# Performance work log

Hardware: AMD Instinct MI355X
Metric: run time of the kernel (lower is better)

Reference implementation:

```python
import jax, jax.numpy as jnp
import numpy as np

D_MODEL = 1024
N_HEADS = 16
D_K = D_MODEL // N_HEADS
NEG_INF = -1.0e9


def setup_inputs() -> dict:
    key = jax.random.key(0)
    ks = jax.random.split(key, 12)
    B, S = 2, 2048
    inp = {
        "q": jax.random.normal(ks[0], (B, S, D_MODEL), dtype=jnp.float32),
        "k": jax.random.normal(ks[1], (B, S, D_MODEL), dtype=jnp.float32),
        "v": jax.random.normal(ks[2], (B, S, D_MODEL), dtype=jnp.float32),
        "mask": jax.random.randint(ks[3], (B, 1, S, S), 0, 2, dtype=jnp.int32),
        "Wq": jax.random.normal(ks[4], (D_MODEL, D_MODEL), dtype=jnp.float32) / np.sqrt(D_MODEL),
        "bq": jnp.zeros((D_MODEL,), dtype=jnp.float32),
        "Wk": jax.random.normal(ks[5], (D_MODEL, D_MODEL), dtype=jnp.float32) / np.sqrt(D_MODEL),
        "bk": jnp.zeros((D_MODEL,), dtype=jnp.float32),
        "Wv": jax.random.normal(ks[6], (D_MODEL, D_MODEL), dtype=jnp.float32) / np.sqrt(D_MODEL),
        "bv": jnp.zeros((D_MODEL,), dtype=jnp.float32),
        "Wo": jax.random.normal(ks[7], (D_MODEL, D_MODEL), dtype=jnp.float32) / np.sqrt(D_MODEL),
        "bo": jnp.zeros((D_MODEL,), dtype=jnp.float32),
    }
    return inp


def _split_heads(x):
    B, S, _ = x.shape
    return x.reshape(B, S, N_HEADS, D_K).transpose(0, 2, 1, 3)  # [B,H,S,Dk]


def reference(q, k, v, mask, Wq, bq, Wk, bk, Wv, bv, Wo, bo):
    # QKV projections (nn.Linear: x @ W.T + b; here W stored as [in,out]-agnostic square)
    query = _split_heads(q @ Wq + bq)
    key_ = _split_heads(k @ Wk + bk)
    value = _split_heads(v @ Wv + bv)

    scale = 1.0 / np.sqrt(D_K).astype(np.float32)
    scores = jnp.einsum("bhqd,bhkd->bhqk", query, key_) * scale  # [B,H,S,S]
    scores = jnp.where(mask == 0, NEG_INF, scores)
    attn = jax.nn.softmax(scores, axis=-1)  # dropout is identity in eval (p=0.0)
    ctx = jnp.einsum("bhqk,bhkd->bhqd", attn, value)  # [B,H,S,Dk]

    B, H, S, Dk = ctx.shape
    ctx = ctx.transpose(0, 2, 1, 3).reshape(B, S, H * Dk)
    return ctx @ Wo + bo
```

## Files before the change

### kernel.cpp

```cpp
#include <hip/hip_runtime.h>
#include <hip/hip_bf16.h>

typedef __bf16 bf16_t;
typedef __bf16 bf16x2 __attribute__((ext_vector_type(2)));
typedef __bf16 bf16x8 __attribute__((ext_vector_type(8)));
typedef float f32x4 __attribute__((ext_vector_type(4)));
typedef float f32x16 __attribute__((ext_vector_type(16)));
typedef int intx4 __attribute__((ext_vector_type(4)));
typedef unsigned int u32;
typedef unsigned long long u64;

#define S_LEN 2048
#define DM 1024
#define NH 16
#define DK 64
#define M_ROWS 4096
#define SCALE_LOG2E 0.1803368801111204f

__device__ __forceinline__ int sw_off(int row, int col) {
  return row * 64 + ((((col >> 3) ^ row) & 7) << 3) + (col & 7);
}

__device__ __forceinline__ bf16x8 cvt8(const float4& a, const float4& b) {
  bf16x8 v;
  v[0] = (__bf16)a.x; v[1] = (__bf16)a.y; v[2] = (__bf16)a.z; v[3] = (__bf16)a.w;
  v[4] = (__bf16)b.x; v[5] = (__bf16)b.y; v[6] = (__bf16)b.z; v[7] = (__bf16)b.w;
  return v;
}

__device__ __forceinline__ void glds16(const bf16_t* g, bf16_t* l) {
  __builtin_amdgcn_global_load_lds(
      (const __attribute__((address_space(1))) void*)g,
      (__attribute__((address_space(3))) void*)l, 16, 0, 0);
}

__device__ __forceinline__ int pk2(float lo, float hi) {
  bf16x2 t;
  t[0] = (__bf16)lo;
  t[1] = (__bf16)hi;
  return __builtin_bit_cast(int, t);
}

__global__ __launch_bounds__(256) void prep(
    const float* __restrict__ q, const float* __restrict__ k,
    const float* __restrict__ v, bf16_t* __restrict__ Xb,
    const float* __restrict__ Wq, const float* __restrict__ Wk,
    const float* __restrict__ Wv, const float* __restrict__ Wo,
    bf16_t* __restrict__ Wt,
    const int* __restrict__ mask, u64* __restrict__ mb)
{
  __shared__ float tile[64][65];
  const int blk = blockIdx.x;
  if (blk < 6144) {
    const int z = blk >> 11;
    const int bx = blk & 2047;
    const float* __restrict__ src = (z == 0) ? q : ((z == 1) ? k : v);
    const size_t idx = ((size_t)bx * 256 + threadIdx.x) * 8;
    const float4 a = *(const float4*)&src[idx];
    const float4 b = *(const float4*)&src[idx + 4];
    *(bf16x8*)&Xb[(size_t)z * M_ROWS * DM + idx] = cvt8(a, b);
  } else if (blk < 7168) {
    const int idx = blk - 6144;
    const int z = idx >> 8, by = (idx >> 4) & 15, bx = idx & 15;
    const float* __restrict__ W = (z == 0) ? Wq : ((z == 1) ? Wk : ((z == 2) ? Wv : Wo));
    bf16_t* __restrict__ out = Wt + (size_t)z * DM * DM;
    const int tx = threadIdx.x & 31, ty = threadIdx.x >> 5;
    const int k0 = bx * 64, n0 = by * 64;
    #pragma unroll
    for (int j = 0; j < 8; ++j) {
      const float2 vv = *(const float2*)&W[(size_t)(k0 + ty + 8 * j) * DM + n0 + tx * 2];
      tile[ty + 8 * j][tx * 2] = vv.x;
      tile[ty + 8 * j][tx * 2 + 1] = vv.y;
    }
    __syncthreads();
    #pragma unroll
    for (int j = 0; j < 8; ++j) {
      const int a = ty + 8 * j;
      bf16x2 p;
      p[0] = (__bf16)tile[tx * 2][a];
      p[1] = (__bf16)tile[tx * 2 + 1][a];
      *(bf16x2*)&out[(size_t)(n0 + a) * DM + k0 + tx * 2] = p;
    }
  } else {
    const int wgl = (blk - 7168) * 4 + (threadIdx.x >> 6);
    const int lane = threadIdx.x & 63;
    const int qq = wgl & 2047;
    const int kw = (wgl >> 11) & 31;
    const int b = wgl >> 16;
    const int val = mask[((size_t)(b * S_LEN + qq)) * S_LEN + kw * 64 + lane];
    const u64 bits = __ballot(val != 0);
    if (lane == 0) mb[wgl] = bits;
  }
}

__device__ __forceinline__ void gemm128_body(
    const bf16_t* __restrict__ A, const bf16_t* __restrict__ Bt,
    const float* __restrict__ bias, const float scale,
    bf16_t* __restrict__ outb, float* __restrict__ outf)
{
  __shared__ __align__(16) bf16_t As[128 * 64];
  __shared__ __align__(16) bf16_t Bs[128 * 64];
  const int t = threadIdx.x, w = t >> 6, L = t & 63, quad = L >> 4, l16 = L & 15;
  const int m0 = blockIdx.x * 128, n0 = blockIdx.y * 128;
  const int mb = 64 * (w & 1), nb = 64 * (w >> 1);
  const int rowS = t >> 3;
  const int ck = (((t & 7) ^ (rowS & 7)) << 3);

  f32x4 acc[4][4] = {};
  for (int k0 = 0; k0 < DM; k0 += 64) {
    __syncthreads();
    #pragma unroll
    for (int j = 0; j < 4; ++j) {
      glds16(&A[(size_t)(m0 + 32 * j + rowS) * DM + k0 + ck],  &As[j * 2048 + t * 8]);
      glds16(&Bt[(size_t)(n0 + 32 * j + rowS) * DM + k0 + ck], &Bs[j * 2048 + t * 8]);
    }
    __syncthreads();
    #pragma unroll
    for (int kk = 0; kk < 2; ++kk) {
      bf16x8 af[4], bfr[4];
      #pragma unroll
      for (int mt = 0; mt < 4; ++mt)
        af[mt] = *(const bf16x8*)&As[sw_off(mb + 16 * mt + l16, kk * 32 + quad * 8)];
      #pragma unroll
      for (int ct = 0; ct < 4; ++ct)
        bfr[ct] = *(const bf16x8*)&Bs[sw_off(nb + 16 * ct + l16, kk * 32 + quad * 8)];
      #pragma unroll
      for (int mt = 0; mt < 4; ++mt)
        #pragma unroll
        for (int ct = 0; ct < 4; ++ct)
          acc[mt][ct] = __builtin_amdgcn_mfma_f32_16x16x32_bf16(af[mt], bfr[ct], acc[mt][ct], 0, 0, 0);
    }
  }
  #pragma unroll
  for (int mt = 0; mt < 4; ++mt)
    #pragma unroll
    for (int ct = 0; ct < 4; ++ct)
      #pragma unroll
      for (int r = 0; r < 4; ++r) {
        const int row = m0 + mb + 16 * mt + quad * 4 + r;
        const int n = n0 + nb + 16 * ct + l16;
        const float val = (acc[mt][ct][r] + bias[n]) * scale;
        if (outb) outb[(size_t)row * DM + n] = (__bf16)val;
        else      outf[(size_t)row * DM + n] = val;
      }
}

__global__ __launch_bounds__(256) void gemm_qkv(
    const bf16_t* __restrict__ Xb, const bf16_t* __restrict__ Wt,
    const float* __restrict__ bq, const float* __restrict__ bk,
    const float* __restrict__ bv, bf16_t* __restrict__ QKVb)
{
  const int z = blockIdx.z;
  gemm128_body(Xb + (size_t)z * M_ROWS * DM, Wt + (size_t)z * DM * DM,
               (z == 0) ? bq : ((z == 1) ? bk : bv),
               (z == 0) ? SCALE_LOG2E : 1.0f,
               QKVb + (size_t)z * M_ROWS * DM, nullptr);
}

__global__ __launch_bounds__(256) void gemm_out(
    const bf16_t* __restrict__ ctx, const bf16_t* __restrict__ Wto,
    const float* __restrict__ bo, float* __restrict__ out)
{
  gemm128_body(ctx, Wto, bo, 1.0f, nullptr, out);
}

__global__ __launch_bounds__(256) void transpV(
    const bf16_t* __restrict__ Vb, bf16_t* __restrict__ Vtw)
{
  __shared__ bf16_t Tr[64 * 72];
  const int t = threadIdx.x;
  const int key0 = blockIdx.x * 64;
  const int bh = blockIdx.y, b = bh >> 4, h = bh & 15;
  const int r = t >> 2, c = (t & 3) * 16;
  const bf16_t* src = &Vb[(size_t)(b * S_LEN + key0 + r) * DM + h * DK + c];
  const bf16x8 v0 = *(const bf16x8*)src;
  const bf16x8 v1 = *(const bf16x8*)(src + 8);
  #pragma unroll
  for (int j = 0; j < 8; ++j) {
    Tr[r * 72 + c + j] = v0[j];
    Tr[r * 72 + c + 8 + j] = v1[j];
  }
  __syncthreads();
  const int dv = t >> 2, kc = (t & 3) * 16;
  bf16_t ov[16];
  #pragma unroll
  for (int j = 0; j < 16; ++j) ov[j] = Tr[(kc + j) * 72 + dv];
  bf16_t* dst = &Vtw[((size_t)bh * DK + dv) * S_LEN + key0 + kc];
  *(bf16x8*)dst = *(bf16x8*)&ov[0];
  *(bf16x8*)(dst + 8) = *(bf16x8*)&ov[8];
}

__global__ __launch_bounds__(512, 2) void attn_kernel(
    const bf16_t* __restrict__ Qb, const bf16_t* __restrict__ Kb,
    const bf16_t* __restrict__ Vtw, const u64* __restrict__ mb,
    bf16_t* __restrict__ ctx)
{
  __shared__ __align__(16) bf16_t KVs[2][4][64 * 64];

  const int t = threadIdx.x, w = t >> 6, L = t & 63;
  const int l31 = L & 31, h5 = L >> 5;
  const int g = blockIdx.x;
  const int xcd = g & 7, slot = g >> 3;
  const int bh = xcd * 4 + (slot >> 3), qt = slot & 7;
  const int q0 = qt * 256;
  const int b = bh >> 4, h = bh & 15;

  const int qr = q0 + 32 * w + l31;
  bf16x8 qf[4];
  {
    const bf16_t* qsrc = &Qb[(size_t)(b * S_LEN + qr) * DM + h * DK + 8 * h5];
    #pragma unroll
    for (int ks = 0; ks < 4; ++ks) qf[ks] = *(const bf16x8*)(qsrc + 16 * ks);
  }

  const int rk = t >> 3;
  const int ck = (t & 7) ^ (rk & 7);
  const bf16_t* pK = &Kb[(size_t)(b * S_LEN + rk) * DM + h * DK + ck * 8];
  const bf16_t* pV = &Vtw[((size_t)bh * DK + rk) * S_LEN + ck * 8];
  const u64* pm = &mb[(size_t)b * 32 * S_LEN + qr];

  f32x16 O[2] = {};
  float l_lane = 0.f;

  auto compute = [&](const bf16_t* __restrict__ Kc, const bf16_t* __restrict__ Vc,
                     u64 mcur) {
    f32x16 s0 = {}, s1 = {};
    #pragma unroll
    for (int ks = 0; ks < 4; ++ks) {
      const bf16x8 kf0 = *(const bf16x8*)&Kc[sw_off(l31, ks * 16 + 8 * h5)];
      const bf16x8 kf1 = *(const bf16x8*)&Kc[sw_off(32 + l31, ks * 16 + 8 * h5)];
      s0 = __builtin_amdgcn_mfma_f32_32x32x16_bf16(kf0, qf[ks], s0, 0, 0, 0);
      s1 = __builtin_amdgcn_mfma_f32_32x32x16_bf16(kf1, qf[ks], s1, 0, 0, 0);
    }
    #pragma unroll
    for (int nt = 0; nt < 2; ++nt) {
      const u32 mm = ((u32)(mcur >> (nt ? 32 : 0))) >> (4 * h5);
      const f32x16 sacc = nt ? s1 : s0;
      float p[16];
      #pragma unroll
      for (int r = 0; r < 16; ++r) {
        const int cb = (r & 3) + 8 * (r >> 2);
        const u32 mr = (u32)(((int)(mm << (31 - cb))) >> 31);
        const float e = __builtin_exp2f(sacc[r]);
        const float pv = __builtin_bit_cast(float, __builtin_bit_cast(u32, e) & mr);
        l_lane += pv;
        p[r] = pv;
      }
      #pragma unroll
      for (int ss = 0; ss < 2; ++ss) {
        const int x0 = pk2(p[8 * ss + 0], p[8 * ss + 1]);
        const int x1 = pk2(p[8 * ss + 2], p[8 * ss + 3]);
        const int y0 = pk2(p[8 * ss + 4], p[8 * ss + 5]);
        const int y1 = pk2(p[8 * ss + 6], p[8 * ss + 7]);
        const auto r0 = __builtin_amdgcn_permlane32_swap(x0, y0, false, false);
        const auto r1 = __builtin_amdgcn_permlane32_swap(x1, y1, false, false);
        intx4 wv;
        wv[0] = r0[0]; wv[1] = r1[0]; wv[2] = r0[1]; wv[3] = r1[1];
        const bf16x8 pf = __builtin_bit_cast(bf16x8, wv);
        const int s4 = 2 * nt + ss;
        const bf16x8 vf0 = *(const bf16x8*)&Vc[sw_off(l31, s4 * 16 + 8 * h5)];
        const bf16x8 vf1 = *(const bf16x8*)&Vc[sw_off(32 + l31, s4 * 16 + 8 * h5)];
        O[0] = __builtin_amdgcn_mfma_f32_32x32x16_bf16(vf0, pf, O[0], 0, 0, 0);
        O[1] = __builtin_amdgcn_mfma_f32_32x32x16_bf16(vf1, pf, O[1], 0, 0, 0);
      }
    }
  };

  bf16x8 k0r = *(const bf16x8*)pK;
  bf16x8 k1r = *(const bf16x8*)(pK + (size_t)64 * DM);
  bf16x8 v0r = *(const bf16x8*)pV;
  bf16x8 v1r = *(const bf16x8*)(pV + 64);
  u64 m0 = pm[0], m1 = pm[S_LEN];
  pK += (size_t)128 * DM; pV += 128; pm += 2 * S_LEN;
  *(bf16x8*)&KVs[0][0][t * 8] = k0r;
  *(bf16x8*)&KVs[0][1][t * 8] = k1r;
  *(bf16x8*)&KVs[0][2][t * 8] = v0r;
  *(bf16x8*)&KVs[0][3][t * 8] = v1r;
  __syncthreads();

  for (int kt = 0; kt < S_LEN / 128; ++kt) {
    const int cur = kt & 1;
    u64 n0 = 0, n1 = 0;
    if (kt + 1 < S_LEN / 128) {
      k0r = *(const bf16x8*)pK;
      k1r = *(const bf16x8*)(pK + (size_t)64 * DM);
      v0r = *(const bf16x8*)pV;
      v1r = *(const bf16x8*)(pV + 64);
      n0 = pm[0]; n1 = pm[S_LEN];
      pK += (size_t)128 * DM; pV += 128; pm += 2 * S_LEN;
    }
    compute(&KVs[cur][0][0], &KVs[cur][2][0], m0);
    compute(&KVs[cur][1][0], &KVs[cur][3][0], m1);
    if (kt + 1 < S_LEN / 128) {
      *(bf16x8*)&KVs[cur ^ 1][0][t * 8] = k0r;
      *(bf16x8*)&KVs[cur ^ 1][1][t * 8] = k1r;
      *(bf16x8*)&KVs[cur ^ 1][2][t * 8] = v0r;
      *(bf16x8*)&KVs[cur ^ 1][3][t * 8] = v1r;
      m0 = n0; m1 = n1;
    }
    __syncthreads();
  }

  const float lsum = l_lane + __shfl_xor(l_lane, 32);
  const float inv = 1.f / lsum;
  bf16_t* sc = &KVs[0][0][0] + (size_t)w * 2048;
  #pragma unroll
  for (int ot = 0; ot < 2; ++ot)
    #pragma unroll
    for (int r = 0; r < 16; ++r) {
      const int dv = 32 * ot + (r & 3) + 8 * (r >> 2) + 4 * h5;
      sc[sw_off(l31, dv)] = (__bf16)(O[ot][r] * inv);
    }
  const int erow = L >> 1, ecol = (L & 1) * 32;
  bf16_t* dst = &ctx[(size_t)(b * S_LEN + q0 + 32 * w + erow) * DM + h * DK + ecol];
  #pragma unroll
  for (int c8 = 0; c8 < 4; ++c8)
    *(bf16x8*)(dst + 8 * c8) = *(const bf16x8*)&sc[sw_off(erow, ecol + 8 * c8)];
}

extern "C" void kernel_launch(void* const* d_in, const int* in_sizes, int n_in,
                              void* d_out, int out_size, void* d_ws, size_t ws_size,
                              hipStream_t stream) {
  const float* q  = (const float*)d_in[0];
  const float* k  = (const float*)d_in[1];
  const float* v  = (const float*)d_in[2];
  const int* mask = (const int*)d_in[3];
  const float* Wq = (const float*)d_in[4];
  const float* bq = (const float*)d_in[5];
  const float* Wk = (const float*)d_in[6];
  const float* bk = (const float*)d_in[7];
  const float* Wv = (const float*)d_in[8];
  const float* bv = (const float*)d_in[9];
  const float* Wo = (const float*)d_in[10];
  const float* bo = (const float*)d_in[11];
  float* out = (float*)d_out;

  const size_t SLICE = (size_t)M_ROWS * DM;
  bf16_t* Xb   = (bf16_t*)d_ws;
  bf16_t* QKVb = Xb + 3 * SLICE;
  bf16_t* Wt   = QKVb + 3 * SLICE;
  u64* mbw     = (u64*)(Wt + (size_t)4 * DM * DM);
  bf16_t* ctx  = Xb;
  bf16_t* Vtw  = Xb + SLICE;

  prep<<<dim3(39936), dim3(256), 0, stream>>>(q, k, v, Xb, Wq, Wk, Wv, Wo, Wt,
                                              mask, mbw);
  gemm_qkv<<<dim3(32, 8, 3), dim3(256), 0, stream>>>(Xb, Wt, bq, bk, bv, QKVb);
  transpV<<<dim3(32, 32), dim3(256), 0, stream>>>(QKVb + 2 * SLICE, Vtw);
  attn_kernel<<<dim3(256), dim3(512), 0, stream>>>(QKVb, QKVb + SLICE, Vtw, mbw, ctx);
  gemm_out<<<dim3(32, 8), dim3(256), 0, stream>>>(ctx, Wt + (size_t)3 * DM * DM, bo, out);
}
```

Baseline: 288.9 us.

## Fuse V transpose into QKV GEMM, vectorize mask packing, retile GEMMs

The separate V-transpose kernel is removed: the V projection now transposes its tile through shared memory and writes the head-transposed layout directly. Mask bit-packing switches from one wavefront ballot per 64 keys to one thread per 64 keys using int4 loads, which cuts the prep grid size. The QKV GEMM drops to a K-step of 32 with an unswizzled LDS layout, and the output GEMM gets a 64x128 tile to launch more blocks. The unswizzled LDS reads may cause bank conflicts, and the smaller K-step doubles the number of barriers.

```diff
diff --git a/kernel.cpp b/kernel.cpp
--- a/kernel.cpp
+++ b/kernel.cpp
@@ -3,6 +3,7 @@
 
 typedef __bf16 bf16_t;
 typedef __bf16 bf16x2 __attribute__((ext_vector_type(2)));
+typedef __bf16 bf16x4 __attribute__((ext_vector_type(4)));
 typedef __bf16 bf16x8 __attribute__((ext_vector_type(8)));
 typedef float f32x4 __attribute__((ext_vector_type(4)));
 typedef float f32x16 __attribute__((ext_vector_type(16)));
@@ -82,55 +83,85 @@
       *(bf16x2*)&out[(size_t)(n0 + a) * DM + k0 + tx * 2] = p;
     }
   } else {
-    const int wgl = (blk - 7168) * 4 + (threadIdx.x >> 6);
-    const int lane = threadIdx.x & 63;
-    const int qq = wgl & 2047;
-    const int kw = (wgl >> 11) & 31;
-    const int b = wgl >> 16;
-    const int val = mask[((size_t)(b * S_LEN + qq)) * S_LEN + kw * 64 + lane];
-    const u64 bits = __ballot(val != 0);
-    if (lane == 0) mb[wgl] = bits;
+    const int g = (blk - 7168) * 256 + threadIdx.x;
+    const int qq = g & 2047;
+    const int kw = (g >> 11) & 31;
+    const int b = g >> 16;
+    const int* src = &mask[((size_t)(b * S_LEN + qq)) * S_LEN + kw * 64];
+    u64 bits = 0;
+    #pragma unroll
+    for (int i = 0; i < 16; ++i) {
+      const int4 m4 = *(const int4*)&src[i * 4];
+      bits |= (u64)(m4.x != 0) << (4 * i);
+      bits |= (u64)(m4.y != 0) << (4 * i + 1);
+      bits |= (u64)(m4.z != 0) << (4 * i + 2);
+      bits |= (u64)(m4.w != 0) << (4 * i + 3);
+    }
+    mb[g] = bits;
   }
 }
 
 __device__ __forceinline__ void gemm128_body(
     const bf16_t* __restrict__ A, const bf16_t* __restrict__ Bt,
     const float* __restrict__ bias, const float scale,
-    bf16_t* __restrict__ outb, float* __restrict__ outf)
-{
-  __shared__ __align__(16) bf16_t As[128 * 64];
-  __shared__ __align__(16) bf16_t Bs[128 * 64];
+    bf16_t* __restrict__ outb, float* __restrict__ outf,
+    bf16_t* __restrict__ vtw)
+{
+  __shared__ __align__(16) bf16_t Smem[128 * 136];
+  bf16_t* As = Smem;
+  bf16_t* Bs = Smem + 4096;
   const int t = threadIdx.x, w = t >> 6, L = t & 63, quad = L >> 4, l16 = L & 15;
   const int m0 = blockIdx.x * 128, n0 = blockIdx.y * 128;
   const int mb = 64 * (w & 1), nb = 64 * (w >> 1);
-  const int rowS = t >> 3;
-  const int ck = (((t & 7) ^ (rowS & 7)) << 3);
+  const int rowS = t >> 2, subS = (t & 3) * 8;
 
   f32x4 acc[4][4] = {};
-  for (int k0 = 0; k0 < DM; k0 += 64) {
-    __syncthreads();
-    #pragma unroll
-    for (int j = 0; j < 4; ++j) {
-      glds16(&A[(size_t)(m0 + 32 * j + rowS) * DM + k0 + ck],  &As[j * 2048 + t * 8]);
-      glds16(&Bt[(size_t)(n0 + 32 * j + rowS) * DM + k0 + ck], &Bs[j * 2048 + t * 8]);
-    }
-    __syncthreads();
-    #pragma unroll
-    for (int kk = 0; kk < 2; ++kk) {
-      bf16x8 af[4], bfr[4];
-      #pragma unroll
-      for (int mt = 0; mt < 4; ++mt)
-        af[mt] = *(const bf16x8*)&As[sw_off(mb + 16 * mt + l16, kk * 32 + quad * 8)];
+  for (int k0 = 0; k0 < DM; k0 += 32) {
+    __syncthreads();
+    glds16(&A[(size_t)(m0 + rowS) * DM + k0 + subS],        &As[t * 8]);
+    glds16(&A[(size_t)(m0 + 64 + rowS) * DM + k0 + subS],   &As[2048 + t * 8]);
+    glds16(&Bt[(size_t)(n0 + rowS) * DM + k0 + subS],       &Bs[t * 8]);
+    glds16(&Bt[(size_t)(n0 + 64 + rowS) * DM + k0 + subS],  &Bs[2048 + t * 8]);
+    __syncthreads();
+    bf16x8 af[4], bfr[4];
+    #pragma unroll
+    for (int mt = 0; mt < 4; ++mt)
+      af[mt] = *(const bf16x8*)&As[(mb + 16 * mt + l16) * 32 + quad * 8];
+    #pragma unroll
+    for (int ct = 0; ct < 4; ++ct)
+      bfr[ct] = *(const bf16x8*)&Bs[(nb + 16 * ct + l16) * 32 + quad * 8];
+    #pragma unroll
+    for (int mt = 0; mt < 4; ++mt)
       #pragma unroll
       for (int ct = 0; ct < 4; ++ct)
-        bfr[ct] = *(const bf16x8*)&Bs[sw_off(nb + 16 * ct + l16, kk * 32 + quad * 8)];
-      #pragma unroll
-      for (int mt = 0; mt < 4; ++mt)
+        acc[mt][ct] = __builtin_amdgcn_mfma_f32_16x16x32_bf16(af[mt], bfr[ct], acc[mt][ct], 0, 0, 0);
+  }
+
+  if (vtw) {
+    __syncthreads();
+    #pragma unroll
+    for (int mt = 0; mt < 4; ++mt)
+      #pragma unroll
+      for (int ct = 0; ct < 4; ++ct) {
+        const int nloc = nb + 16 * ct + l16;
+        const int mloc0 = mb + 16 * mt + quad * 4;
+        bf16x4 pk;
         #pragma unroll
-        for (int ct = 0; ct < 4; ++ct)
-          acc[mt][ct] = __builtin_amdgcn_mfma_f32_16x16x32_bf16(af[mt], bfr[ct], acc[mt][ct], 0, 0, 0);
-    }
-  }
+        for (int r = 0; r < 4; ++r)
+          pk[r] = (__bf16)(acc[mt][ct][r] + bias[n0 + nloc]);
+        *(bf16x4*)&Smem[nloc * 136 + mloc0] = pk;
+      }
+    __syncthreads();
+    const int nloc = t >> 1, mh = (t & 1) * 64;
+    const int n = n0 + nloc, h = n >> 6, dv = n & 63;
+    const int b = m0 >> 11, key0 = (m0 & 2047) + mh;
+    bf16_t* dst = &vtw[(((size_t)(b * NH + h)) * DK + dv) * S_LEN + key0];
+    #pragma unroll
+    for (int j = 0; j < 8; ++j)
+      *(bf16x8*)(dst + 8 * j) = *(const bf16x8*)&Smem[nloc * 136 + mh + 8 * j];
+    return;
+  }
+
   #pragma unroll
   for (int mt = 0; mt < 4; ++mt)
     #pragma unroll
@@ -148,46 +179,58 @@
 __global__ __launch_bounds__(256) void gemm_qkv(
     const bf16_t* __restrict__ Xb, const bf16_t* __restrict__ Wt,
     const float* __restrict__ bq, const float* __restrict__ bk,
-    const float* __restrict__ bv, bf16_t* __restrict__ QKVb)
+    const float* __restrict__ bv, bf16_t* __restrict__ QKVb,
+    bf16_t* __restrict__ Vtw)
 {
   const int z = blockIdx.z;
   gemm128_body(Xb + (size_t)z * M_ROWS * DM, Wt + (size_t)z * DM * DM,
                (z == 0) ? bq : ((z == 1) ? bk : bv),
                (z == 0) ? SCALE_LOG2E : 1.0f,
-               QKVb + (size_t)z * M_ROWS * DM, nullptr);
+               (z == 2) ? nullptr : QKVb + (size_t)z * M_ROWS * DM, nullptr,
+               (z == 2) ? Vtw : nullptr);
 }
 
 __global__ __launch_bounds__(256) void gemm_out(
-    const bf16_t* __restrict__ ctx, const bf16_t* __restrict__ Wto,
-    const float* __restrict__ bo, float* __restrict__ out)
-{
-  gemm128_body(ctx, Wto, bo, 1.0f, nullptr, out);
-}
-
-__global__ __launch_bounds__(256) void transpV(
-    const bf16_t* __restrict__ Vb, bf16_t* __restrict__ Vtw)
-{
-  __shared__ bf16_t Tr[64 * 72];
-  const int t = threadIdx.x;
-  const int key0 = blockIdx.x * 64;
-  const int bh = blockIdx.y, b = bh >> 4, h = bh & 15;
-  const int r = t >> 2, c = (t & 3) * 16;
-  const bf16_t* src = &Vb[(size_t)(b * S_LEN + key0 + r) * DM + h * DK + c];
-  const bf16x8 v0 = *(const bf16x8*)src;
-  const bf16x8 v1 = *(const bf16x8*)(src + 8);
+    const bf16_t* __restrict__ A, const bf16_t* __restrict__ Bt,
+    const float* __restrict__ bias, float* __restrict__ outf)
+{
+  __shared__ __align__(16) bf16_t As[64 * 32];
+  __shared__ __align__(16) bf16_t Bs[128 * 32];
+  const int t = threadIdx.x, w = t >> 6, L = t & 63, quad = L >> 4, l16 = L & 15;
+  const int m0 = blockIdx.x * 64, n0 = blockIdx.y * 128;
+  const int nb = 32 * w;
+  const int rowS = t >> 2, subS = (t & 3) * 8;
+
+  f32x4 acc[4][2] = {};
+  for (int k0 = 0; k0 < DM; k0 += 32) {
+    __syncthreads();
+    glds16(&A[(size_t)(m0 + rowS) * DM + k0 + subS],        &As[t * 8]);
+    glds16(&Bt[(size_t)(n0 + rowS) * DM + k0 + subS],       &Bs[t * 8]);
+    glds16(&Bt[(size_t)(n0 + 64 + rowS) * DM + k0 + subS],  &Bs[2048 + t * 8]);
+    __syncthreads();
+    bf16x8 af[4], bfr[2];
+    #pragma unroll
+    for (int mt = 0; mt < 4; ++mt)
+      af[mt] = *(const bf16x8*)&As[(16 * mt + l16) * 32 + quad * 8];
+    #pragma unroll
+    for (int ct = 0; ct < 2; ++ct)
+      bfr[ct] = *(const bf16x8*)&Bs[(nb + 16 * ct + l16) * 32 + quad * 8];
+    #pragma unroll
+    for (int mt = 0; mt < 4; ++mt)
+      #pragma unroll
+      for (int ct = 0; ct < 2; ++ct)
+        acc[mt][ct] = __builtin_amdgcn_mfma_f32_16x16x32_bf16(af[mt], bfr[ct], acc[mt][ct], 0, 0, 0);
+  }
   #pragma unroll
-  for (int j = 0; j < 8; ++j) {
-    Tr[r * 72 + c + j] = v0[j];
-    Tr[r * 72 + c + 8 + j] = v1[j];
-  }
-  __syncthreads();
-  const int dv = t >> 2, kc = (t & 3) * 16;
-  bf16_t ov[16];
-  #pragma unroll
-  for (int j = 0; j < 16; ++j) ov[j] = Tr[(kc + j) * 72 + dv];
-  bf16_t* dst = &Vtw[((size_t)bh * DK + dv) * S_LEN + key0 + kc];
-  *(bf16x8*)dst = *(bf16x8*)&ov[0];
-  *(bf16x8*)(dst + 8) = *(bf16x8*)&ov[8];
+  for (int mt = 0; mt < 4; ++mt)
+    #pragma unroll
+    for (int ct = 0; ct < 2; ++ct)
+      #pragma unroll
+      for (int r = 0; r < 4; ++r) {
+        const int row = m0 + 16 * mt + quad * 4 + r;
+        const int n = n0 + nb + 16 * ct + l16;
+        outf[(size_t)row * DM + n] = acc[mt][ct][r] + bias[n];
+      }
 }
 
 __global__ __launch_bounds__(512, 2) void attn_kernel(
@@ -341,12 +384,11 @@
   bf16_t* Wt   = QKVb + 3 * SLICE;
   u64* mbw     = (u64*)(Wt + (size_t)4 * DM * DM);
   bf16_t* ctx  = Xb;
-  bf16_t* Vtw  = Xb + SLICE;
-
-  prep<<<dim3(39936), dim3(256), 0, stream>>>(q, k, v, Xb, Wq, Wk, Wv, Wo, Wt,
-                                              mask, mbw);
-  gemm_qkv<<<dim3(32, 8, 3), dim3(256), 0, stream>>>(Xb, Wt, bq, bk, bv, QKVb);
-  transpV<<<dim3(32, 32), dim3(256), 0, stream>>>(QKVb + 2 * SLICE, Vtw);
+  bf16_t* Vtw  = QKVb + 2 * SLICE;
+
+  prep<<<dim3(7680), dim3(256), 0, stream>>>(q, k, v, Xb, Wq, Wk, Wv, Wo, Wt,
+                                             mask, mbw);
+  gemm_qkv<<<dim3(32, 8, 3), dim3(256), 0, stream>>>(Xb, Wt, bq, bk, bv, QKVb, Vtw);
   attn_kernel<<<dim3(256), dim3(512), 0, stream>>>(QKVb, QKVb + SLICE, Vtw, mbw, ctx);
-  gemm_out<<<dim3(32, 8), dim3(256), 0, stream>>>(ctx, Wt + (size_t)3 * DM * DM, bo, out);
-}
+  gemm_out<<<dim3(64, 8), dim3(256), 0, stream>>>(ctx, Wt + (size_t)3 * DM * DM, bo, out);
+}
```

After: 281.5 us. -2.6%, faster.
